# Kernel tuning notes

Measured on AMD Instinct MI355X. Metric: run time of the kernel, lower is better.

Reference implementation:

```python
import jax, jax.numpy as jnp
import numpy as np

B, S, D = 4, 2048, 1024
HALF_PI = np.float32(np.pi / 2.0)


def setup_inputs() -> dict:
    key = jax.random.key(0)
    ks = jax.random.split(key, 12)
    std = np.float32(0.02)
    def w(k):
        return jax.random.normal(k, (D, D), dtype=jnp.float32) * std
    return {
        "x": jax.random.normal(ks[0], (B, S, D), dtype=jnp.float32),
        "W_q": w(ks[1]), "b_q": jnp.zeros((D,), jnp.float32),
        "W_k": w(ks[2]), "b_k": jnp.zeros((D,), jnp.float32),
        "W_v": w(ks[3]), "b_v": jnp.zeros((D,), jnp.float32),
        "W_t": w(ks[4]), "b_t": jnp.zeros((D,), jnp.float32),
        "W_o": w(ks[5]), "b_o": jnp.zeros((D,), jnp.float32),
        "entangle_strength": jnp.float32(0.5),
    }


def reference(x, W_q, b_q, W_k, b_k, W_v, b_v, W_t, b_t, W_o, b_o, entangle_strength):
    scale = jnp.float32(np.sqrt(D))
    Q = x @ W_q + b_q          # [B,S,D]
    K = x @ W_k + b_k
    V = x @ W_v + b_v
    # theta in [0, pi/2]; r = cos(2*theta)
    theta_q = jax.nn.sigmoid(Q @ W_t + b_t) * HALF_PI
    theta_k = jax.nn.sigmoid(K @ W_t + b_t) * HALF_PI
    r_q = jnp.cos(2.0 * theta_q)
    r_k = jnp.cos(2.0 * theta_k)
    classical = jnp.einsum("bqd,bkd->bqk", Q, K) / scale
    quantum = jnp.einsum("bqd,bkd->bqk", r_q, r_k) * entangle_strength
    attn_weights = jax.nn.softmax(classical + quantum, axis=-1)  # [B,S,S]
    # dropout: eval mode -> identity
    out = jnp.einsum("bqk,bkd->bqd", attn_weights, V)
    out = out @ W_o + b_o
    return out, attn_weights
```

## Files before the change

kernel.cpp:

```cpp
#include <hip/hip_runtime.h>
#include <cstdint>

typedef unsigned short u16;
typedef __attribute__((ext_vector_type(8))) short bf16x8;
typedef __attribute__((ext_vector_type(4))) float f32x4;

__device__ __forceinline__ u16 f2b(float x) {
  unsigned u = __float_as_uint(x);
  u += 0x7FFFu + ((u >> 16) & 1u);
  return (u16)(u >> 16);
}

__device__ __forceinline__ void gload16(const void* g, void* l) {
  __builtin_amdgcn_global_load_lds(
      (const __attribute__((address_space(1))) void*)g,
      (__attribute__((address_space(3))) void*)l, 16, 0, 0);
}

template <int N>
__device__ __forceinline__ void vmwait() {
  if constexpr (N == 0) asm volatile("s_waitcnt vmcnt(0)" ::: "memory");
  else if constexpr (N == 3) asm volatile("s_waitcnt vmcnt(3)" ::: "memory");
  else if constexpr (N == 4) asm volatile("s_waitcnt vmcnt(4)" ::: "memory");
  else if constexpr (N == 6) asm volatile("s_waitcnt vmcnt(6)" ::: "memory");
  else if constexpr (N == 8) asm volatile("s_waitcnt vmcnt(8)" ::: "memory");
}

template <int L>
__device__ __forceinline__ void stage_half(const u16* __restrict__ G,
                                           long long ld, int kb,
                                           u16* Ldst, int tid) {
#pragma unroll
  for (int j = 0; j < L; ++j) {
    const int P = j * 512 + tid;
    const int r = P >> 3, c = P & 7;
    gload16(G + (long long)r * ld + kb + ((c ^ (r & 7)) << 3), Ldst + P * 8);
  }
}

__device__ __forceinline__ bf16x8 fr8(const u16* R, int row, int chunk) {
  return *(const bf16x8*)(R + row * 64 + ((chunk ^ (row & 7)) << 3));
}

template <int FM, int MODE>
__device__ __forceinline__ void tile_body(
    u16* cur, u16* oth, const u16* GA_lo, const u16* GA_hi,
    const u16* GB_lo, const u16* GB_hi, long long lda, long long ldb,
    int kb1, int kb2, int wm, int wn, int lr, int cA, int tid,
    f32x4 (&acc)[2][2][FM][2]) {
  constexpr int LA = FM / 2, LB = 2;
  constexpr int AH = 2048 * FM, BH = 8192;
  const u16* Alo = cur;
  const u16* Ahi = cur + AH;
  const u16* Blo = cur + 2 * AH;
  const u16* Bhi = cur + 2 * AH + BH;
  const int ar = wm * (FM * 16) + lr;
  const int br = wn * 32 + lr;
  bf16x8 a[FM][2], b[2][2];

#pragma unroll
  for (int f = 0; f < FM; ++f) {
    a[f][0] = fr8(Alo, ar + f * 16, cA);
    a[f][1] = fr8(Alo, ar + f * 16, 4 + cA);
  }
#pragma unroll
  for (int g = 0; g < 2; ++g) {
    b[g][0] = fr8(Blo, br + g * 16, cA);
    b[g][1] = fr8(Blo, br + g * 16, 4 + cA);
  }
  if constexpr (MODE < 2) stage_half<LA>(GA_hi, lda, kb1, oth + AH, tid);
  if constexpr (FM == 4) asm volatile("s_waitcnt lgkmcnt(8)" ::: "memory");
  if constexpr (MODE < 2) vmwait<2 * LA + 2>(); else vmwait<0>();
  __builtin_amdgcn_s_barrier();
  asm volatile("s_waitcnt lgkmcnt(0)" ::: "memory");
  __builtin_amdgcn_s_setprio(1);
#pragma unroll
  for (int kh = 0; kh < 2; ++kh)
#pragma unroll
    for (int f = 0; f < FM; ++f)
#pragma unroll
      for (int g = 0; g < 2; ++g)
        acc[0][0][f][g] = __builtin_amdgcn_mfma_f32_16x16x32_bf16(
            a[f][kh], b[g][kh], acc[0][0][f][g], 0, 0, 0);
  __builtin_amdgcn_s_setprio(0);
  __builtin_amdgcn_s_barrier();

#pragma unroll
  for (int g = 0; g < 2; ++g) {
    b[g][0] = fr8(Bhi, br + g * 16, cA);
    b[g][1] = fr8(Bhi, br + g * 16, 4 + cA);
  }
  if constexpr (MODE < 2) stage_half<LB>(GB_hi, ldb, kb1, oth + 2 * AH + BH, tid);
  __builtin_amdgcn_s_barrier();
  asm volatile("s_waitcnt lgkmcnt(0)" ::: "memory");
  __builtin_amdgcn_s_setprio(1);
#pragma unroll
  for (int kh = 0; kh < 2; ++kh)
#pragma unroll
    for (int f = 0; f < FM; ++f)
#pragma unroll
      for (int g = 0; g < 2; ++g)
        acc[0][1][f][g] = __builtin_amdgcn_mfma_f32_16x16x32_bf16(
            a[f][kh], b[g][kh], acc[0][1][f][g], 0, 0, 0);
  __builtin_amdgcn_s_setprio(0);
  __builtin_amdgcn_s_barrier();

#pragma unroll
  for (int f = 0; f < FM; ++f) {
    a[f][0] = fr8(Ahi, ar + f * 16, cA);
    a[f][1] = fr8(Ahi, ar + f * 16, 4 + cA);
  }
#pragma unroll
  for (int g = 0; g < 2; ++g) {
    b[g][0] = fr8(Blo, br + g * 16, cA);
    b[g][1] = fr8(Blo, br + g * 16, 4 + cA);
  }
  if constexpr (MODE == 0) stage_half<LA>(GA_lo, lda, kb2, cur, tid);
  if constexpr (FM == 4) asm volatile("s_waitcnt lgkmcnt(8)" ::: "memory");
  __builtin_amdgcn_s_barrier();
  asm volatile("s_waitcnt lgkmcnt(0)" ::: "memory");
  __builtin_amdgcn_s_setprio(1);
#pragma unroll
  for (int kh = 0; kh < 2; ++kh)
#pragma unroll
    for (int f = 0; f < FM; ++f)
#pragma unroll
      for (int g = 0; g < 2; ++g)
        acc[1][0][f][g] = __builtin_amdgcn_mfma_f32_16x16x32_bf16(
            a[f][kh], b[g][kh], acc[1][0][f][g], 0, 0, 0);
  __builtin_amdgcn_s_setprio(0);
  __builtin_amdgcn_s_barrier();

#pragma unroll
  for (int g = 0; g < 2; ++g) {
    b[g][0] = fr8(Bhi, br + g * 16, cA);
    b[g][1] = fr8(Bhi, br + g * 16, 4 + cA);
  }
  if constexpr (MODE == 0) stage_half<LB>(GB_lo, ldb, kb2, cur + 2 * AH, tid);
  if constexpr (MODE == 0) vmwait<2 * LA + 4>();
  else if constexpr (MODE == 1) vmwait<LA + 2>();
  __builtin_amdgcn_s_barrier();
  asm volatile("s_waitcnt lgkmcnt(0)" ::: "memory");
  __builtin_amdgcn_s_setprio(1);
#pragma unroll
  for (int kh = 0; kh < 2; ++kh)
#pragma unroll
    for (int f = 0; f < FM; ++f)
#pragma unroll
      for (int g = 0; g < 2; ++g)
        acc[1][1][f][g] = __builtin_amdgcn_mfma_f32_16x16x32_bf16(
            a[f][kh], b[g][kh], acc[1][1][f][g], 0, 0, 0);
  __builtin_amdgcn_s_setprio(0);
  __builtin_amdgcn_s_barrier();
}

template <int EPI, int FM>
__global__ __launch_bounds__(512, 2) void g8q(
    const u16* __restrict__ A, long long lda, long long sAz,
    const u16* __restrict__ B, long long ldb, long long sBz,
    void* __restrict__ C0, void* __restrict__ C1, void* __restrict__ C2,
    long long ldc, long long sCz, int K,
    const float* __restrict__ b0, const float* __restrict__ b1,
    const float* __restrict__ b2, float preScale, const float* __restrict__ esp) {
  constexpr int BM = 64 * FM;
  constexpr int LA = FM / 2, LB = 2;
  constexpr int AH = 2048 * FM, BH = 8192;
  constexpr int BUFU = 2 * AH + 2 * BH;
  __shared__ __align__(16) u16 lds[2 * BUFU];
  u16* buf0 = lds;
  u16* buf1 = lds + BUFU;

  const int gx = gridDim.x, S = gx * gridDim.y;
  const int hw = blockIdx.y * gx + blockIdx.x;
  const int l = (hw & 7) * (S >> 3) + (hw >> 3);
  const int bx = l % gx, by = l / gx;
  const int z = blockIdx.z;
  const long long tM = (long long)by * BM;
  const long long tN = (long long)bx * 256;
  const u16* Ab = A + z * sAz + tM * lda;
  const u16* Bb = B + z * sBz + tN * ldb;
  const u16* GA_lo = Ab;
  const u16* GA_hi = Ab + (long long)(BM / 2) * lda;
  const u16* GB_lo = Bb;
  const u16* GB_hi = Bb + 128 * ldb;
  const int tid = threadIdx.x;
  const int NT = K >> 6;

  stage_half<LA>(GA_lo, lda, 0, buf0, tid);
  stage_half<LB>(GB_lo, ldb, 0, buf0 + 2 * AH, tid);
  stage_half<LA>(GA_hi, lda, 0, buf0 + AH, tid);
  stage_half<LB>(GB_hi, ldb, 0, buf0 + 2 * AH + BH, tid);
  stage_half<LA>(GA_lo, lda, 64, buf1, tid);
  stage_half<LB>(GB_lo, ldb, 64, buf1 + 2 * AH, tid);
  vmwait<2 * LA + 4>();
  __builtin_amdgcn_s_barrier();

  const int wid = tid >> 6, lane = tid & 63;
  const int wm = wid >> 2, wn = wid & 3;
  const int lr = lane & 15, cA = lane >> 4;
  f32x4 acc[2][2][FM][2] = {};

  for (int t = 0; t + 2 < NT; t += 2) {
    tile_body<FM, 0>(buf0, buf1, GA_lo, GA_hi, GB_lo, GB_hi, lda, ldb,
                     (t + 1) * 64, (t + 2) * 64, wm, wn, lr, cA, tid, acc);
    tile_body<FM, 0>(buf1, buf0, GA_lo, GA_hi, GB_lo, GB_hi, lda, ldb,
                     (t + 2) * 64, (t + 3) * 64, wm, wn, lr, cA, tid, acc);
  }
  tile_body<FM, 1>(buf0, buf1, GA_lo, GA_hi, GB_lo, GB_hi, lda, ldb,
                   (NT - 1) * 64, 0, wm, wn, lr, cA, tid, acc);
  tile_body<FM, 2>(buf1, buf0, GA_lo, GA_hi, GB_lo, GB_hi, lda, ldb,
                   0, 0, wm, wn, lr, cA, tid, acc);

  const int rr = (lane >> 4) << 2;
  float ps = preScale, mul = 1.0f;
  if constexpr (EPI == 1) {
    ps = (z == 0) ? preScale : 1.0f;
    mul = (z == 0) ? esp[0] : 1.0f;
  }
#pragma unroll
  for (int mh = 0; mh < 2; ++mh) {
#pragma unroll
    for (int nh = 0; nh < 2; ++nh) {
#pragma unroll
      for (int f = 0; f < FM; ++f) {
#pragma unroll
        for (int g = 0; g < 2; ++g) {
          const int col = (int)tN + nh * 128 + wn * 32 + g * 16 + lr;
          const f32x4 vv = acc[mh][nh][f][g];
#pragma unroll
          for (int r = 0; r < 4; ++r) {
            const long long row =
                tM + mh * (BM / 2) + wm * (FM * 16) + f * 16 + rr + r;
            const float v = vv[r];
            if constexpr (EPI == 0) {
              const int gg = col >> 10, cc = col & 1023;
              if (gg == 0)      ((u16*)C0)[row * 2048 + cc] = f2b((v + b0[cc]) * 0.03125f);
              else if (gg == 1) ((u16*)C1)[row * 2048 + cc] = f2b(v + b1[cc]);
              else              ((u16*)C2)[row * 1024 + cc] = f2b(v + b2[cc]);
            } else if constexpr (EPI == 1) {
              const float tt = v * ps + b0[col];
              const float sg = 1.f / (1.f + __expf(-tt));
              ((u16*)C0)[z * sCz + row * ldc + col] = f2b(mul * cospif(sg));
            } else if constexpr (EPI == 2) {
              ((u16*)C0)[z * sCz + row * ldc + col] = f2b(v);
            } else if constexpr (EPI == 3) {
              ((float*)C0)[z * sCz + row * ldc + col] = v + b0[col];
            } else {
              ((float*)C0)[z * sCz + row * ldc + col] = v;
            }
          }
        }
      }
    }
  }
}

__global__ __launch_bounds__(256) void softmax_rows(float* __restrict__ L,
                                                    u16* __restrict__ AB) {
  const long long row = blockIdx.x;
  float4* p4 = (float4*)(L + row * 2048);
  const int tid = threadIdx.x;
  float4 a = p4[tid], b = p4[tid + 256];
  float m = fmaxf(fmaxf(fmaxf(a.x, a.y), fmaxf(a.z, a.w)),
                  fmaxf(fmaxf(b.x, b.y), fmaxf(b.z, b.w)));
#pragma unroll
  for (int o = 32; o > 0; o >>= 1) m = fmaxf(m, __shfl_xor(m, o));
  __shared__ float rmax[4], rsum[4];
  const int wid = tid >> 6, lane = tid & 63;
  if (lane == 0) rmax[wid] = m;
  __syncthreads();
  m = fmaxf(fmaxf(rmax[0], rmax[1]), fmaxf(rmax[2], rmax[3]));
  a.x = __expf(a.x - m); a.y = __expf(a.y - m);
  a.z = __expf(a.z - m); a.w = __expf(a.w - m);
  b.x = __expf(b.x - m); b.y = __expf(b.y - m);
  b.z = __expf(b.z - m); b.w = __expf(b.w - m);
  float s = a.x + a.y + a.z + a.w + b.x + b.y + b.z + b.w;
#pragma unroll
  for (int o = 32; o > 0; o >>= 1) s += __shfl_xor(s, o);
  if (lane == 0) rsum[wid] = s;
  __syncthreads();
  s = rsum[0] + rsum[1] + rsum[2] + rsum[3];
  const float inv = 1.0f / s;
  a.x *= inv; a.y *= inv; a.z *= inv; a.w *= inv;
  b.x *= inv; b.y *= inv; b.z *= inv; b.w *= inv;
  p4[tid] = a;
  p4[tid + 256] = b;
  ushort4* o4 = (ushort4*)(AB + row * 2048);
  o4[tid]       = make_ushort4(f2b(a.x), f2b(a.y), f2b(a.z), f2b(a.w));
  o4[tid + 256] = make_ushort4(f2b(b.x), f2b(b.y), f2b(b.z), f2b(b.w));
}

__global__ __launch_bounds__(256) void cvt_x(const float* __restrict__ X,
                                             u16* __restrict__ XB) {
  const int i = blockIdx.x * 256 + threadIdx.x;
  float4 v = ((const float4*)X)[i];
  ((ushort4*)XB)[i] = make_ushort4(f2b(v.x), f2b(v.y), f2b(v.z), f2b(v.w));
}

__global__ void cvt_w(const float* __restrict__ W0, const float* __restrict__ W1,
                      const float* __restrict__ W2, const float* __restrict__ W3,
                      const float* __restrict__ W4, u16* __restrict__ WT) {
  __shared__ float t[32][33];
  const int z = blockIdx.z;
  const float* W = (z == 0) ? W0 : (z == 1) ? W1 : (z == 2) ? W2 : (z == 3) ? W3 : W4;
  u16* D = WT + (long long)z * 1024 * 1024;
  const int c0 = blockIdx.x * 32, r0 = blockIdx.y * 32;
  const int tx = threadIdx.x, ty = threadIdx.y;
#pragma unroll
  for (int i = 0; i < 4; ++i)
    t[ty + i * 8][tx] = W[(long long)(r0 + ty + i * 8) * 1024 + c0 + tx];
  __syncthreads();
#pragma unroll
  for (int i = 0; i < 4; ++i)
    D[(long long)(c0 + ty + i * 8) * 1024 + r0 + tx] = f2b(t[tx][ty + i * 8]);
}

__global__ void transpose_v(const u16* __restrict__ Vb, u16* __restrict__ VT) {
  __shared__ u16 t[32][33];
  const int b = blockIdx.z;
  const u16* V = Vb + (long long)b * 2048 * 1024;
  u16* O = VT + (long long)b * 1024 * 2048;
  const int d0 = blockIdx.x * 32, s0 = blockIdx.y * 32;
  const int tx = threadIdx.x, ty = threadIdx.y;
#pragma unroll
  for (int i = 0; i < 4; ++i)
    t[ty + i * 8][tx] = V[(long long)(s0 + ty + i * 8) * 1024 + d0 + tx];
  __syncthreads();
#pragma unroll
  for (int i = 0; i < 4; ++i)
    O[(long long)(d0 + ty + i * 8) * 2048 + s0 + tx] = t[tx][ty + i * 8];
}

extern "C" void kernel_launch(void* const* d_in, const int* in_sizes, int n_in,
                              void* d_out, int out_size, void* d_ws,
                              size_t ws_size, hipStream_t stream) {
  const float* x  = (const float*)d_in[0];
  const float* Wq = (const float*)d_in[1];
  const float* bq = (const float*)d_in[2];
  const float* Wk = (const float*)d_in[3];
  const float* bk = (const float*)d_in[4];
  const float* Wv = (const float*)d_in[5];
  const float* bv = (const float*)d_in[6];
  const float* Wt = (const float*)d_in[7];
  const float* bt = (const float*)d_in[8];
  const float* Wo = (const float*)d_in[9];
  const float* bo = (const float*)d_in[10];
  const float* es = (const float*)d_in[11];

  char* ws = (char*)d_ws;
  u16* WT   = (u16*)(ws);
  u16* XB   = (u16*)(ws + 10485760);
  u16* Qcat = (u16*)(ws + 27262976);
  u16* Kcat = Qcat + 16777216;
  u16* Vb   = (u16*)(ws + 94371840);
  u16* VT   = (u16*)(ws + 111149056);
  u16* WtT  = WT + 3 * 1048576;
  u16* WoT  = WT + 4 * 1048576;
  u16* ATT  = Qcat;
  u16* AV   = XB;

  float* outO = (float*)d_out;
  float* outA = outO + 8388608;

  cvt_x<<<8192, 256, 0, stream>>>(x, XB);
  cvt_w<<<dim3(32, 32, 5), dim3(32, 8), 0, stream>>>(Wq, Wk, Wv, Wt, Wo, WT);
  g8q<0, 4><<<dim3(12, 32, 1), 512, 0, stream>>>(
      XB, 1024, 0, WT, 1024, 0, Qcat, Kcat, Vb, 0, 0, 1024, bq, bk, bv,
      1.f, nullptr);
  g8q<1, 4><<<dim3(4, 32, 2), 512, 0, stream>>>(
      Qcat, 2048, 16777216LL, WtT, 1024, 0, Qcat + 1024, nullptr, nullptr,
      2048, 16777216LL, 1024, bt, nullptr, nullptr, 32.f, es);
  transpose_v<<<dim3(32, 64, 4), dim3(32, 8), 0, stream>>>(Vb, VT);
  g8q<4, 4><<<dim3(8, 8, 4), 512, 0, stream>>>(
      Qcat, 2048, 4194304LL, Kcat, 2048, 4194304LL, outA, nullptr, nullptr,
      2048, 4194304LL, 2048, nullptr, nullptr, nullptr, 1.f, nullptr);
  softmax_rows<<<8192, 256, 0, stream>>>(outA, ATT);
  g8q<2, 4><<<dim3(4, 8, 4), 512, 0, stream>>>(
      ATT, 2048, 4194304LL, VT, 2048, 2097152LL, AV, nullptr, nullptr,
      1024, 2097152LL, 2048, nullptr, nullptr, nullptr, 1.f, nullptr);
  g8q<3, 4><<<dim3(4, 32, 1), 512, 0, stream>>>(
      AV, 1024, 0, WoT, 1024, 0, outO, nullptr, nullptr,
      1024, 0, 1024, bo, nullptr, nullptr, 1.f, nullptr);
}
```

Measured before the change: 368.4 us.

## Add 128x128 double-buffered GEMM kernel for QKV, AV and output projections

Introduces a smaller-tile 128x128 bf16 MFMA GEMM kernel (256 threads, BK=32, double-buffered LDS with swizzled rows and a grid remap for locality). It replaces the larger-tile g8q kernel for the fused QKV projection, attention-times-V and the output projection. The aim is more blocks and better occupancy and CU balance on these moderately sized GEMMs. In exchange, operand reuse per tile drops and each K step carries its own barrier.

```diff
diff --git a/kernel.cpp b/kernel.cpp
--- a/kernel.cpp
+++ b/kernel.cpp
@@ -15,6 +15,10 @@
   __builtin_amdgcn_global_load_lds(
       (const __attribute__((address_space(1))) void*)g,
       (__attribute__((address_space(3))) void*)l, 16, 0, 0);
+}
+
+__device__ __forceinline__ void vmwait0() {
+  asm volatile("s_waitcnt vmcnt(0)" ::: "memory");
 }
 
 template <int N>
@@ -40,6 +44,104 @@
 
 __device__ __forceinline__ bf16x8 fr8(const u16* R, int row, int chunk) {
   return *(const bf16x8*)(R + row * 64 + ((chunk ^ (row & 7)) << 3));
+}
+
+__device__ __forceinline__ void stage128(const u16* __restrict__ G,
+                                         long long ld, int kb,
+                                         u16* Ldst, int tid) {
+#pragma unroll
+  for (int j = 0; j < 2; ++j) {
+    const int P = j * 256 + tid;
+    const int r = P >> 2, c = P & 3;
+    gload16(G + (long long)r * ld + kb + ((c ^ (r & 3)) << 3), Ldst + P * 8);
+  }
+}
+
+__device__ __forceinline__ bf16x8 fr4(const u16* R, int row, int chunk) {
+  return *(const bf16x8*)(R + row * 32 + ((chunk ^ (row & 3)) << 3));
+}
+
+template <int EPI>
+__global__ __launch_bounds__(256, 4) void e2p(
+    const u16* __restrict__ A, long long lda, long long sAz,
+    const u16* __restrict__ B, long long ldb, long long sBz,
+    void* __restrict__ C0, void* __restrict__ C1, void* __restrict__ C2,
+    long long ldc, long long sCz, int K,
+    const float* __restrict__ b0, const float* __restrict__ b1,
+    const float* __restrict__ b2) {
+  constexpr int HALF = 4096;
+  constexpr int BUFU = 2 * HALF;
+  __shared__ __align__(16) u16 lds[2 * BUFU];
+
+  const int gx = gridDim.x, S = gx * gridDim.y;
+  const int hw = blockIdx.y * gx + blockIdx.x;
+  const int l = (hw & 7) * (S >> 3) + (hw >> 3);
+  const int bx = l % gx, by = l / gx;
+  const int z = blockIdx.z;
+  const long long tM = (long long)by * 128;
+  const long long tN = (long long)bx * 128;
+  const u16* GA = A + z * sAz + tM * lda;
+  const u16* GB = B + z * sBz + tN * ldb;
+  const int tid = threadIdx.x;
+  const int NT = K >> 5;
+
+  stage128(GA, lda, 0, lds, tid);
+  stage128(GB, ldb, 0, lds + HALF, tid);
+  vmwait0();
+  __builtin_amdgcn_s_barrier();
+
+  const int wid = tid >> 6, lane = tid & 63;
+  const int wr = (wid >> 1) * 64, wc = (wid & 1) * 64;
+  const int lr = lane & 15, cA = lane >> 4;
+  f32x4 acc[4][4] = {};
+
+  for (int t = 0; t < NT; ++t) {
+    const u16* cur = lds + (t & 1) * BUFU;
+    if (t + 1 < NT) {
+      u16* nxt = lds + ((t + 1) & 1) * BUFU;
+      stage128(GA, lda, (t + 1) * 32, nxt, tid);
+      stage128(GB, ldb, (t + 1) * 32, nxt + HALF, tid);
+    }
+    bf16x8 a[4], b[4];
+#pragma unroll
+    for (int m = 0; m < 4; ++m) a[m] = fr4(cur, wr + m * 16 + lr, cA);
+#pragma unroll
+    for (int n = 0; n < 4; ++n) b[n] = fr4(cur + HALF, wc + n * 16 + lr, cA);
+#pragma unroll
+    for (int m = 0; m < 4; ++m)
+#pragma unroll
+      for (int n = 0; n < 4; ++n)
+        acc[m][n] = __builtin_amdgcn_mfma_f32_16x16x32_bf16(a[m], b[n],
+                                                            acc[m][n], 0, 0, 0);
+    if (t + 1 < NT) {
+      vmwait0();
+      __builtin_amdgcn_s_barrier();
+    }
+  }
+
+  const int rr = (lane >> 4) << 2;
+#pragma unroll
+  for (int m = 0; m < 4; ++m) {
+#pragma unroll
+    for (int n = 0; n < 4; ++n) {
+      const int col = (int)tN + wc + n * 16 + lr;
+#pragma unroll
+      for (int r = 0; r < 4; ++r) {
+        const long long row = tM + wr + m * 16 + rr + r;
+        const float v = acc[m][n][r];
+        if constexpr (EPI == 0) {
+          const int gg = col >> 10, cc = col & 1023;
+          if (gg == 0)      ((u16*)C0)[row * 2048 + cc] = f2b((v + b0[cc]) * 0.03125f);
+          else if (gg == 1) ((u16*)C1)[row * 2048 + cc] = f2b(v + b1[cc]);
+          else              ((u16*)C2)[row * 1024 + cc] = f2b(v + b2[cc]);
+        } else if constexpr (EPI == 2) {
+          ((u16*)C0)[z * sCz + row * ldc + col] = f2b(v);
+        } else {
+          ((float*)C0)[z * sCz + row * ldc + col] = v + b0[col];
+        }
+      }
+    }
+  }
 }
 
 template <int FM, int MODE>
@@ -232,19 +334,10 @@
             const long long row =
                 tM + mh * (BM / 2) + wm * (FM * 16) + f * 16 + rr + r;
             const float v = vv[r];
-            if constexpr (EPI == 0) {
-              const int gg = col >> 10, cc = col & 1023;
-              if (gg == 0)      ((u16*)C0)[row * 2048 + cc] = f2b((v + b0[cc]) * 0.03125f);
-              else if (gg == 1) ((u16*)C1)[row * 2048 + cc] = f2b(v + b1[cc]);
-              else              ((u16*)C2)[row * 1024 + cc] = f2b(v + b2[cc]);
-            } else if constexpr (EPI == 1) {
+            if constexpr (EPI == 1) {
               const float tt = v * ps + b0[col];
               const float sg = 1.f / (1.f + __expf(-tt));
               ((u16*)C0)[z * sCz + row * ldc + col] = f2b(mul * cospif(sg));
-            } else if constexpr (EPI == 2) {
-              ((u16*)C0)[z * sCz + row * ldc + col] = f2b(v);
-            } else if constexpr (EPI == 3) {
-              ((float*)C0)[z * sCz + row * ldc + col] = v + b0[col];
             } else {
               ((float*)C0)[z * sCz + row * ldc + col] = v;
             }
@@ -364,9 +457,8 @@
 
   cvt_x<<<8192, 256, 0, stream>>>(x, XB);
   cvt_w<<<dim3(32, 32, 5), dim3(32, 8), 0, stream>>>(Wq, Wk, Wv, Wt, Wo, WT);
-  g8q<0, 4><<<dim3(12, 32, 1), 512, 0, stream>>>(
-      XB, 1024, 0, WT, 1024, 0, Qcat, Kcat, Vb, 0, 0, 1024, bq, bk, bv,
-      1.f, nullptr);
+  e2p<0><<<dim3(24, 64, 1), 256, 0, stream>>>(
+      XB, 1024, 0, WT, 1024, 0, Qcat, Kcat, Vb, 0, 0, 1024, bq, bk, bv);
   g8q<1, 4><<<dim3(4, 32, 2), 512, 0, stream>>>(
       Qcat, 2048, 16777216LL, WtT, 1024, 0, Qcat + 1024, nullptr, nullptr,
       2048, 16777216LL, 1024, bt, nullptr, nullptr, 32.f, es);
@@ -375,10 +467,10 @@
       Qcat, 2048, 4194304LL, Kcat, 2048, 4194304LL, outA, nullptr, nullptr,
       2048, 4194304LL, 2048, nullptr, nullptr, nullptr, 1.f, nullptr);
   softmax_rows<<<8192, 256, 0, stream>>>(outA, ATT);
-  g8q<2, 4><<<dim3(4, 8, 4), 512, 0, stream>>>(
+  e2p<2><<<dim3(8, 16, 4), 256, 0, stream>>>(
       ATT, 2048, 4194304LL, VT, 2048, 2097152LL, AV, nullptr, nullptr,
-      1024, 2097152LL, 2048, nullptr, nullptr, nullptr, 1.f, nullptr);
-  g8q<3, 4><<<dim3(4, 32, 1), 512, 0, stream>>>(
+      1024, 2097152LL, 2048, nullptr, nullptr, nullptr);
+  e2p<3><<<dim3(8, 64, 1), 256, 0, stream>>>(
       AV, 1024, 0, WoT, 1024, 0, outO, nullptr, nullptr,
-      1024, 0, 1024, bo, nullptr, nullptr, 1.f, nullptr);
-}
+      1024, 0, 1024, bo, nullptr, nullptr);
+}
```

Result: faster. 337.4 us (-8.4%).
